# Kernel tuning notes

Measured on AMD Instinct MI355X. Metric: run time of the kernel, lower is better.

## Reference

```python
import jax, jax.numpy as jnp
import numpy as np

B, C, H, W = 4, 64, 64, 64


def setup_inputs() -> dict:
    key = jax.random.key(0)
    k1, k2, k3, k4, k5 = jax.random.split(key, 5)
    return {
        "x": jax.random.normal(k1, (B, C, H, W), dtype=jnp.float32),
        "w_qkv": jax.random.normal(k2, (3 * C, C), dtype=jnp.float32) * (1.0 / np.sqrt(C)),
        "b_qkv": jax.random.normal(k3, (3 * C,), dtype=jnp.float32) * 0.02,
        "w_proj": jax.random.normal(k4, (C, C), dtype=jnp.float32) * (1.0 / np.sqrt(C)),
        "b_proj": jax.random.normal(k5, (C,), dtype=jnp.float32) * 0.02,
    }


def reference(x, w_qkv, b_qkv, w_proj, b_proj):
    b, c, h, w = x.shape
    xf = x.reshape(b, c, h * w)                                  # [B, C, N]
    # 1x1 Conv1d == per-position linear over channels
    qkv = jnp.einsum('oc,bcn->bon', w_qkv, xf) + b_qkv[None, :, None]  # [B, 3C, N]
    q, k, v = jnp.split(qkv, 3, axis=1)                          # each [B, C, N]
    scores = jnp.einsum('bcn,bcm->bnm', q, k) / (c ** 0.5)       # [B, N, N]
    attn = jax.nn.softmax(scores, axis=-1)
    out = jnp.einsum('bcm,bnm->bcn', v, attn)                    # [B, C, N]
    out = jnp.einsum('oc,bcn->bon', w_proj, out) + b_proj[None, :, None]
    return out.reshape(b, c, h, w) + x
```

## Files before the change

kernel.cpp:

```cpp
#include <hip/hip_runtime.h>

typedef __bf16 bf16x8 __attribute__((ext_vector_type(8)));
typedef __bf16 bf16x4 __attribute__((ext_vector_type(4)));
typedef float f32x4 __attribute__((ext_vector_type(4)));
typedef short s16x4 __attribute__((ext_vector_type(4)));

#define NB 4
#define NC 64
#define NN 4096
#define SPLIT 8

#define QSCALE (0.125f * 1.44269504088896340736f)

#if __has_builtin(__builtin_amdgcn_exp2f)
#define EXP2(x) __builtin_amdgcn_exp2f(x)
#else
#define EXP2(x) exp2f(x)
#endif

__global__ __launch_bounds__(256) void qkv_kernel(
    const float* __restrict__ x, const float* __restrict__ wqkv,
    const float* __restrict__ bqkv,
    __bf16* __restrict__ Qg, __bf16* __restrict__ Kg, __bf16* __restrict__ Vg)
{
  const int tid = threadIdx.x;
  const int wave = tid >> 6;
  const int lane = tid & 63;
  const int quad = lane >> 4;
  const int l16 = lane & 15;
  const int b = blockIdx.y;
  const int tsel = blockIdx.z;
  const int n0 = blockIdx.x * 128 + wave * 32;
  const float wscale = (tsel == 0) ? QSCALE : 1.0f;

  bf16x8 wf[4][2];
#pragma unroll
  for (int ot = 0; ot < 4; ot++) {
#pragma unroll
    for (int ch = 0; ch < 2; ch++) {
      const float* wp =
          wqkv + (size_t)(tsel * 64 + ot * 16 + l16) * 64 + ch * 32 + quad * 8;
      const float4 w0 = *(const float4*)wp;
      const float4 w1 = *(const float4*)(wp + 4);
      bf16x8 f;
      f[0] = (__bf16)(w0.x * wscale); f[1] = (__bf16)(w0.y * wscale);
      f[2] = (__bf16)(w0.z * wscale); f[3] = (__bf16)(w0.w * wscale);
      f[4] = (__bf16)(w1.x * wscale); f[5] = (__bf16)(w1.y * wscale);
      f[6] = (__bf16)(w1.z * wscale); f[7] = (__bf16)(w1.w * wscale);
      wf[ot][ch] = f;
    }
  }
  float bv[4];
#pragma unroll
  for (int ot = 0; ot < 4; ot++)
    bv[ot] = bqkv[tsel * 64 + ot * 16 + l16] * wscale;

#pragma unroll
  for (int nt = 0; nt < 2; nt++) {
    const int nb = n0 + nt * 16 + l16;

    bf16x8 xf[2];
#pragma unroll
    for (int ch = 0; ch < 2; ch++) {
      float v[8];
#pragma unroll
      for (int j = 0; j < 8; j++)
        v[j] = x[(size_t)(b * 64 + ch * 32 + quad * 8 + j) * NN + nb];
      bf16x8 f;
#pragma unroll
      for (int j = 0; j < 8; j++) f[j] = (__bf16)v[j];
      xf[ch] = f;
    }

#pragma unroll
    for (int ot = 0; ot < 4; ot++) {
      f32x4 acc = (f32x4){bv[ot], bv[ot], bv[ot], bv[ot]};
      acc = __builtin_amdgcn_mfma_f32_16x16x32_bf16(xf[0], wf[ot][0], acc, 0, 0, 0);
      acc = __builtin_amdgcn_mfma_f32_16x16x32_bf16(xf[1], wf[ot][1], acc, 0, 0, 0);

      if (tsel < 2) {
        __bf16* dst = (tsel == 0) ? Qg : Kg;
#pragma unroll
        for (int r = 0; r < 4; r++)
          dst[(size_t)(b * NN + n0 + nt * 16 + quad * 4 + r) * 64 + ot * 16 + l16] =
              (__bf16)acc[r];
      } else {
        bf16x4 pv;
#pragma unroll
        for (int r = 0; r < 4; r++) pv[r] = (__bf16)acc[r];
        *(bf16x4*)(Vg + (size_t)(b * 64 + ot * 16 + l16) * NN +
                   n0 + nt * 16 + quad * 4) = pv;
      }
    }
  }
}

__global__ __launch_bounds__(256) void flash_kernel(
    const __bf16* __restrict__ Q, const __bf16* __restrict__ K,
    const __bf16* __restrict__ V, const float* __restrict__ wproj,
    __bf16* __restrict__ Opart, float* __restrict__ lpart)
{
  const int b = blockIdx.y;
  const int s = blockIdx.z;
  const int tid = threadIdx.x;
  const int wave = tid >> 6;
  const int lane = tid & 63;
  const int quad = lane >> 4;
  const int l16 = lane & 15;

  __shared__ __bf16 Kt[64 * 72];
  __shared__ __bf16 Vt[64 * 72];

  const int q0 = blockIdx.x * 128 + wave * 32;

  bf16x8 qf[2][2];
#pragma unroll
  for (int qt = 0; qt < 2; qt++) {
    const __bf16* qrow = Q + ((size_t)(b * NN + q0 + qt * 16 + l16)) * 64;
    qf[qt][0] = *(const bf16x8*)(qrow + quad * 8);
    qf[qt][1] = *(const bf16x8*)(qrow + 32 + quad * 8);
  }

  f32x4 acc[2][4];
#pragma unroll
  for (int qt = 0; qt < 2; qt++)
#pragma unroll
    for (int ct = 0; ct < 4; ct++) acc[qt][ct] = (f32x4){0.f, 0.f, 0.f, 0.f};
  float l[2] = {0.f, 0.f};

  const int kbeg = s * (NN / SPLIT);
  const int kend = kbeg + (NN / SPLIT);
#pragma unroll 1
  for (int kt0 = kbeg; kt0 < kend; kt0 += 64) {
    __syncthreads();
#pragma unroll
    for (int it = 0; it < 2; it++) {
      const int chunk = tid + it * 256;
      const int row = chunk >> 3, col8 = (chunk & 7) * 8;
      *(bf16x8*)(&Kt[row * 72 + col8]) =
          *(const bf16x8*)(K + ((size_t)(b * NN + kt0 + row)) * 64 + col8);
      *(bf16x8*)(&Vt[row * 72 + col8]) =
          *(const bf16x8*)(V + ((size_t)(b * 64 + row)) * NN + kt0 + col8);
    }
    __syncthreads();

    s16x4 pk[4][2];
#pragma unroll
    for (int t = 0; t < 4; t++) {
      const bf16x8 kf0 = *(const bf16x8*)(&Kt[(t * 16 + l16) * 72 + quad * 8]);
      const bf16x8 kf1 = *(const bf16x8*)(&Kt[(t * 16 + l16) * 72 + 32 + quad * 8]);
#pragma unroll
      for (int qt = 0; qt < 2; qt++) {
        f32x4 z = (f32x4){0.f, 0.f, 0.f, 0.f};
        z = __builtin_amdgcn_mfma_f32_16x16x32_bf16(kf0, qf[qt][0], z, 0, 0, 0);
        z = __builtin_amdgcn_mfma_f32_16x16x32_bf16(kf1, qf[qt][1], z, 0, 0, 0);
        const float p0 = EXP2(z[0]), p1 = EXP2(z[1]);
        const float p2 = EXP2(z[2]), p3 = EXP2(z[3]);
        l[qt] += (p0 + p1) + (p2 + p3);
        bf16x4 pv;
        pv[0] = (__bf16)p0; pv[1] = (__bf16)p1;
        pv[2] = (__bf16)p2; pv[3] = (__bf16)p3;
        pk[t][qt] = __builtin_bit_cast(s16x4, pv);
      }
    }

#pragma unroll
    for (int kg = 0; kg < 4; kg++) {
#pragma unroll
      for (int ct = 0; ct < 4; ct++) {
        const bf16x4 va =
            *(const bf16x4*)(&Vt[(ct * 16 + l16) * 72 + kg * 16 + quad * 4]);
        const s16x4 a = __builtin_bit_cast(s16x4, va);
        acc[0][ct] = __builtin_amdgcn_mfma_f32_16x16x16bf16_1k(
            a, pk[kg][0], acc[0][ct], 0, 0, 0);
        acc[1][ct] = __builtin_amdgcn_mfma_f32_16x16x16bf16_1k(
            a, pk[kg][1], acc[1][ct], 0, 0, 0);
      }
    }
  }

#pragma unroll
  for (int qt = 0; qt < 2; qt++) {
    float lr = l[qt];
    lr += __shfl_xor(lr, 16);
    lr += __shfl_xor(lr, 32);
    if (quad == 0)
      lpart[((size_t)(s * NB + b)) * NN + q0 + qt * 16 + l16] = lr;
  }

  s16x4 ob[2][4];
#pragma unroll
  for (int qt = 0; qt < 2; qt++)
#pragma unroll
    for (int ch = 0; ch < 4; ch++) {
      bf16x4 t;
#pragma unroll
      for (int r = 0; r < 4; r++) t[r] = (__bf16)acc[qt][ch][r];
      ob[qt][ch] = __builtin_bit_cast(s16x4, t);
    }

#pragma unroll
  for (int cot = 0; cot < 4; cot++) {
    f32x4 po[2];
    po[0] = (f32x4){0.f, 0.f, 0.f, 0.f};
    po[1] = (f32x4){0.f, 0.f, 0.f, 0.f};
#pragma unroll
    for (int ch = 0; ch < 4; ch++) {
      const float4 wv =
          *(const float4*)&wproj[(cot * 16 + l16) * 64 + ch * 16 + quad * 4];
      bf16x4 wb;
      wb[0] = (__bf16)wv.x; wb[1] = (__bf16)wv.y;
      wb[2] = (__bf16)wv.z; wb[3] = (__bf16)wv.w;
      const s16x4 a = __builtin_bit_cast(s16x4, wb);
      po[0] = __builtin_amdgcn_mfma_f32_16x16x16bf16_1k(a, ob[0][ch], po[0], 0, 0, 0);
      po[1] = __builtin_amdgcn_mfma_f32_16x16x16bf16_1k(a, ob[1][ch], po[1], 0, 0, 0);
    }
#pragma unroll
    for (int qt = 0; qt < 2; qt++)
#pragma unroll
      for (int r = 0; r < 4; r++)
        Opart[(((size_t)(s * NB + b)) * 64 + cot * 16 + quad * 4 + r) * NN +
              q0 + qt * 16 + l16] = (__bf16)po[qt][r];
  }
}

__global__ __launch_bounds__(256) void combine_kernel(
    const __bf16* __restrict__ Opart, const float* __restrict__ lpart,
    const float* __restrict__ bproj, const float* __restrict__ x,
    float* __restrict__ out)
{
  const int b = blockIdx.y;
  const int n0 = blockIdx.x * 32;
  const int tid = threadIdx.x;

  __shared__ float linv[32];
  if (tid < 32) {
    float lt = 0.f;
#pragma unroll
    for (int s = 0; s < SPLIT; s++)
      lt += lpart[((size_t)(s * NB + b)) * NN + n0 + tid];
    linv[tid] = 1.0f / lt;
  }
  __syncthreads();

  const int c = tid >> 2;
  const int n8 = (tid & 3) * 8;

  float o[8];
#pragma unroll
  for (int j = 0; j < 8; j++) o[j] = 0.f;
#pragma unroll
  for (int s = 0; s < SPLIT; s++) {
    const bf16x8 v = *(const bf16x8*)(
        Opart + (((size_t)(s * NB + b)) * 64 + c) * NN + n0 + n8);
#pragma unroll
    for (int j = 0; j < 8; j++) o[j] += (float)v[j];
  }

  const float bb = bproj[c];
  const float4 li0 = *(const float4*)&linv[n8];
  const float4 li1 = *(const float4*)&linv[n8 + 4];
  const size_t base = ((size_t)(b * 64 + c)) * NN + n0 + n8;
  const float4 x0 = *(const float4*)&x[base];
  const float4 x1 = *(const float4*)&x[base + 4];
  float4 r0, r1;
  r0.x = o[0] * li0.x + bb + x0.x;  r0.y = o[1] * li0.y + bb + x0.y;
  r0.z = o[2] * li0.z + bb + x0.z;  r0.w = o[3] * li0.w + bb + x0.w;
  r1.x = o[4] * li1.x + bb + x1.x;  r1.y = o[5] * li1.y + bb + x1.y;
  r1.z = o[6] * li1.z + bb + x1.z;  r1.w = o[7] * li1.w + bb + x1.w;
  *(float4*)&out[base] = r0;
  *(float4*)&out[base + 4] = r1;
}

extern "C" void kernel_launch(void* const* d_in, const int* in_sizes, int n_in,
                              void* d_out, int out_size, void* d_ws, size_t ws_size,
                              hipStream_t stream) {
  const float* x     = (const float*)d_in[0];
  const float* wqkv  = (const float*)d_in[1];
  const float* bqkv  = (const float*)d_in[2];
  const float* wproj = (const float*)d_in[3];
  const float* bproj = (const float*)d_in[4];
  float* out = (float*)d_out;

  char* ws = (char*)d_ws;
  __bf16* Q     = (__bf16*)(ws);
  __bf16* K     = (__bf16*)(ws + (2u << 20));
  __bf16* V     = (__bf16*)(ws + (4u << 20));
  __bf16* Opart = (__bf16*)(ws + (6u << 20));
  float*  lpart = (float*)(ws + (23u << 20));

  qkv_kernel<<<dim3(32, NB, 3), 256, 0, stream>>>(x, wqkv, bqkv, Q, K, V);
  flash_kernel<<<dim3(32, NB, SPLIT), 256, 0, stream>>>(Q, K, V, wproj,
                                                        Opart, lpart);
  combine_kernel<<<dim3(128, NB), 256, 0, stream>>>(Opart, lpart, bproj, x,
                                                    out);
}
```

Baseline: 113.5 us.

## Fuse split-K combine into flash kernel via last-block atomic counter

Removes the separate combine kernel launch. Each flash block increments a per-(batch, query tile) atomic counter after writing its partial output, and the last of the SPLIT blocks reduces all partials, normalizes, adds bias and the residual, and writes the final output. The counters are zeroed inside the qkv kernel so no extra memset launch is needed. This saves one launch and its gap but serializes the reduction onto the tail blocks and adds fences and atomics.

```diff
diff --git a/kernel.cpp b/kernel.cpp
--- a/kernel.cpp
+++ b/kernel.cpp
@@ -21,7 +21,8 @@
 __global__ __launch_bounds__(256) void qkv_kernel(
     const float* __restrict__ x, const float* __restrict__ wqkv,
     const float* __restrict__ bqkv,
-    __bf16* __restrict__ Qg, __bf16* __restrict__ Kg, __bf16* __restrict__ Vg)
+    __bf16* __restrict__ Qg, __bf16* __restrict__ Kg, __bf16* __restrict__ Vg,
+    int* __restrict__ cnt)
 {
   const int tid = threadIdx.x;
   const int wave = tid >> 6;
@@ -32,6 +33,9 @@
   const int tsel = blockIdx.z;
   const int n0 = blockIdx.x * 128 + wave * 32;
   const float wscale = (tsel == 0) ? QSCALE : 1.0f;
+
+  if (blockIdx.x == 0 && blockIdx.y == 0 && blockIdx.z == 0 && tid < NB * 32)
+    cnt[tid] = 0;
 
   bf16x8 wf[4][2];
 #pragma unroll
@@ -98,8 +102,11 @@
 __global__ __launch_bounds__(256) void flash_kernel(
     const __bf16* __restrict__ Q, const __bf16* __restrict__ K,
     const __bf16* __restrict__ V, const float* __restrict__ wproj,
-    __bf16* __restrict__ Opart, float* __restrict__ lpart)
+    const float* __restrict__ bproj, const float* __restrict__ x,
+    __bf16* __restrict__ Opart, float* __restrict__ lpart,
+    int* __restrict__ cnt, float* __restrict__ out)
 {
+  const int xblk = blockIdx.x;
   const int b = blockIdx.y;
   const int s = blockIdx.z;
   const int tid = threadIdx.x;
@@ -110,8 +117,9 @@
 
   __shared__ __bf16 Kt[64 * 72];
   __shared__ __bf16 Vt[64 * 72];
-
-  const int q0 = blockIdx.x * 128 + wave * 32;
+  __shared__ int lastFlag;
+
+  const int q0 = xblk * 128 + wave * 32;
 
   bf16x8 qf[2][2];
 #pragma unroll
@@ -222,54 +230,58 @@
         Opart[(((size_t)(s * NB + b)) * 64 + cot * 16 + quad * 4 + r) * NN +
               q0 + qt * 16 + l16] = (__bf16)po[qt][r];
   }
-}
-
-__global__ __launch_bounds__(256) void combine_kernel(
-    const __bf16* __restrict__ Opart, const float* __restrict__ lpart,
-    const float* __restrict__ bproj, const float* __restrict__ x,
-    float* __restrict__ out)
-{
-  const int b = blockIdx.y;
-  const int n0 = blockIdx.x * 32;
-  const int tid = threadIdx.x;
-
-  __shared__ float linv[32];
-  if (tid < 32) {
-    float lt = 0.f;
-#pragma unroll
-    for (int s = 0; s < SPLIT; s++)
-      lt += lpart[((size_t)(s * NB + b)) * NN + n0 + tid];
-    linv[tid] = 1.0f / lt;
-  }
+
   __syncthreads();
-
+  if (tid == 0) {
+    __threadfence();
+    lastFlag = (atomicAdd(&cnt[b * 32 + xblk], 1) == SPLIT - 1);
+  }
+  __syncthreads();
+  if (!lastFlag) return;
+  __threadfence();
+
+  float* linv = (float*)Kt;
   const int c = tid >> 2;
-  const int n8 = (tid & 3) * 8;
-
-  float o[8];
-#pragma unroll
-  for (int j = 0; j < 8; j++) o[j] = 0.f;
-#pragma unroll
-  for (int s = 0; s < SPLIT; s++) {
-    const bf16x8 v = *(const bf16x8*)(
-        Opart + (((size_t)(s * NB + b)) * 64 + c) * NN + n0 + n8);
-#pragma unroll
-    for (int j = 0; j < 8; j++) o[j] += (float)v[j];
-  }
-
-  const float bb = bproj[c];
-  const float4 li0 = *(const float4*)&linv[n8];
-  const float4 li1 = *(const float4*)&linv[n8 + 4];
-  const size_t base = ((size_t)(b * 64 + c)) * NN + n0 + n8;
-  const float4 x0 = *(const float4*)&x[base];
-  const float4 x1 = *(const float4*)&x[base + 4];
-  float4 r0, r1;
-  r0.x = o[0] * li0.x + bb + x0.x;  r0.y = o[1] * li0.y + bb + x0.y;
-  r0.z = o[2] * li0.z + bb + x0.z;  r0.w = o[3] * li0.w + bb + x0.w;
-  r1.x = o[4] * li1.x + bb + x1.x;  r1.y = o[5] * li1.y + bb + x1.y;
-  r1.z = o[6] * li1.z + bb + x1.z;  r1.w = o[7] * li1.w + bb + x1.w;
-  *(float4*)&out[base] = r0;
-  *(float4*)&out[base + 4] = r1;
+  const int n8o = (tid & 3) * 8;
+
+#pragma unroll 1
+  for (int pass = 0; pass < 4; pass++) {
+    const int n0 = xblk * 128 + pass * 32;
+    __syncthreads();
+    if (tid < 32) {
+      float lt = 0.f;
+#pragma unroll
+      for (int ss = 0; ss < SPLIT; ss++)
+        lt += lpart[((size_t)(ss * NB + b)) * NN + n0 + tid];
+      linv[tid] = 1.0f / lt;
+    }
+    __syncthreads();
+
+    float o[8];
+#pragma unroll
+    for (int j = 0; j < 8; j++) o[j] = 0.f;
+#pragma unroll
+    for (int ss = 0; ss < SPLIT; ss++) {
+      const bf16x8 v = *(const bf16x8*)(
+          Opart + (((size_t)(ss * NB + b)) * 64 + c) * NN + n0 + n8o);
+#pragma unroll
+      for (int j = 0; j < 8; j++) o[j] += (float)v[j];
+    }
+
+    const float bb = bproj[c];
+    const float4 li0 = *(const float4*)&linv[n8o];
+    const float4 li1 = *(const float4*)&linv[n8o + 4];
+    const size_t base = ((size_t)(b * 64 + c)) * NN + n0 + n8o;
+    const float4 x0 = *(const float4*)&x[base];
+    const float4 x1 = *(const float4*)&x[base + 4];
+    float4 r0, r1;
+    r0.x = o[0] * li0.x + bb + x0.x;  r0.y = o[1] * li0.y + bb + x0.y;
+    r0.z = o[2] * li0.z + bb + x0.z;  r0.w = o[3] * li0.w + bb + x0.w;
+    r1.x = o[4] * li1.x + bb + x1.x;  r1.y = o[5] * li1.y + bb + x1.y;
+    r1.z = o[6] * li1.z + bb + x1.z;  r1.w = o[7] * li1.w + bb + x1.w;
+    *(float4*)&out[base] = r0;
+    *(float4*)&out[base + 4] = r1;
+  }
 }
 
 extern "C" void kernel_launch(void* const* d_in, const int* in_sizes, int n_in,
@@ -288,10 +300,9 @@
   __bf16* V     = (__bf16*)(ws + (4u << 20));
   __bf16* Opart = (__bf16*)(ws + (6u << 20));
   float*  lpart = (float*)(ws + (23u << 20));
-
-  qkv_kernel<<<dim3(32, NB, 3), 256, 0, stream>>>(x, wqkv, bqkv, Q, K, V);
-  flash_kernel<<<dim3(32, NB, SPLIT), 256, 0, stream>>>(Q, K, V, wproj,
-                                                        Opart, lpart);
-  combine_kernel<<<dim3(128, NB), 256, 0, stream>>>(Opart, lpart, bproj, x,
-                                                    out);
+  int*    cnt   = (int*)(ws + (24u << 20));
+
+  qkv_kernel<<<dim3(32, NB, 3), 256, 0, stream>>>(x, wqkv, bqkv, Q, K, V, cnt);
+  flash_kernel<<<dim3(32, NB, SPLIT), 256, 0, stream>>>(
+      Q, K, V, wproj, bproj, x, Opart, lpart, cnt, out);
 }
```

After: 170.1 us. +49.9%, slower.
